# Kernel optimization log

Hardware: AMD Instinct MI355X
Metric: run time of the kernel (lower is better)

## Reference

```python
import jax, jax.numpy as jnp
import numpy as np

B, T, DIM = 1, 2048, 1024
NUM_HEADS, HEAD_DIM = 8, 128
ATTN_SCALE = 0.12


def _rms_norm(x):
    # F.rms_norm(x, x.size(-1)) with no weight; eps defaults to machine eps
    eps = jnp.asarray(jnp.finfo(x.dtype).eps, x.dtype)
    return x * jax.lax.rsqrt(jnp.mean(x * x, axis=-1, keepdims=True) + eps)


def _rotary_tables(seq_len, head_dim):
    # (1/1024) ** linspace(0,1,head_dim//4), then pad with head_dim//4 zeros
    freq = (1.0 / 1024.0) ** jnp.linspace(0.0, 1.0, head_dim // 4, dtype=jnp.float32)
    ang = jnp.concatenate([freq, jnp.zeros(head_dim // 4, jnp.float32)])  # [hd/2]
    theta = jnp.arange(seq_len, dtype=jnp.float32)[:, None] * ang[None, :]  # [T, hd/2]
    return jnp.cos(theta), jnp.sin(theta)


def _apply_rotary(x, cos, sin):
    # x: [B, T, H, hd]
    x1, x2 = jnp.split(x.astype(jnp.float32), 2, axis=-1)
    c = cos[None, :, None, :]
    s = sin[None, :, None, :]
    y1 = x1 * c + x2 * s
    y2 = -x1 * s + x2 * c
    return jnp.concatenate([y1, y2], axis=-1).astype(x.dtype)


def setup_inputs() -> dict:
    key = jax.random.key(0)
    ks = jax.random.split(key, 5)
    bound = (3.0 ** 0.5) * 0.5 * DIM ** (-0.5)
    x = jax.random.normal(ks[0], (B, T, DIM), jnp.float32)
    ve = jax.random.normal(ks[1], (B, T, NUM_HEADS * HEAD_DIM), jnp.float32)
    qkv_w = jax.random.uniform(ks[2], (3, NUM_HEADS * HEAD_DIM, DIM), jnp.float32, -bound, bound)
    lambdas = jnp.array([0.5, 0.5], jnp.float32)
    # original zero-inits c_proj; use small random weight so the output is nontrivial
    c_proj_w = jax.random.uniform(ks[3], (DIM, NUM_HEADS * HEAD_DIM), jnp.float32, -bound, bound)
    return {"x": x, "ve": ve, "qkv_w": qkv_w, "lambdas": lambdas, "c_proj_w": c_proj_w}


def reference(x, ve, qkv_w, lambdas, c_proj_w):
    Bx, Tx, D = x.shape
    H, hd = NUM_HEADS, HEAD_DIM
    # fused QKV projection: weight [3*H*hd, D]
    qkv = x @ qkv_w.reshape(3 * H * hd, D).T            # [B, T, 3*H*hd]
    qkv = qkv.reshape(Bx, Tx, 3 * H, hd)
    q, k, v = jnp.split(qkv, 3, axis=-2)                # each [B, T, H, hd]
    q, k = _rms_norm(q), _rms_norm(k)
    cos, sin = _rotary_tables(Tx, hd)
    q, k = _apply_rotary(q, cos, sin), _apply_rotary(k, cos, sin)
    v = lambdas[0] * v + lambdas[1] * ve.reshape(v.shape)
    att = jnp.einsum('bthd,bshd->bhts', q, k) * ATTN_SCALE
    causal = jnp.tril(jnp.ones((Tx, Tx), bool))
    att = jnp.where(causal[None, None], att, -jnp.inf)
    att = jax.nn.softmax(att, axis=-1)
    y = jnp.einsum('bhts,bshd->bthd', att, v).reshape(Bx, Tx, H * hd)
    return y @ c_proj_w.T
```

## Files before the change

### kernel.cpp

```cpp
#include <hip/hip_runtime.h>


typedef __attribute__((ext_vector_type(8))) short short8;
typedef __attribute__((ext_vector_type(4))) short short4b;
typedef __attribute__((ext_vector_type(4))) float fx4;
typedef __attribute__((ext_vector_type(8))) unsigned short ushort8;
typedef __attribute__((ext_vector_type(4))) unsigned short ushort4v;
typedef __attribute__((ext_vector_type(2))) unsigned short ushort2v;
typedef __attribute__((ext_vector_type(4))) float float4v;

#define T_SEQ 2048
#define NH 8
#define HD 128

__device__ __forceinline__ unsigned short f2bf(float f) {
  union { float f; unsigned u; } v; v.f = f;
  unsigned u = v.u;
  u += 0x7fffu + ((u >> 16) & 1u);
  return (unsigned short)(u >> 16);
}
__device__ __forceinline__ short bf_t(float f) {
  union { float f; unsigned u; } v; v.f = f;
  return (short)(v.u >> 16);
}
__device__ __forceinline__ float bf2f(unsigned short h) {
  union { unsigned u; float f; } v; v.u = ((unsigned)h) << 16;
  return v.f;
}

typedef __attribute__((address_space(1))) unsigned int glb_u32;
typedef __attribute__((address_space(3))) unsigned int lds_u32;
__device__ __forceinline__ void gl_lds16(const unsigned short* g, unsigned short* l) {
  __builtin_amdgcn_global_load_lds((const glb_u32*)g, (lds_u32*)l, 16, 0, 0);
}

__global__ __launch_bounds__(256) void cast3_kernel(
    const float* __restrict__ x, const float* __restrict__ w1,
    const float* __restrict__ w2, unsigned short* __restrict__ o) {
  long q = (long)blockIdx.x * 256 + threadIdx.x;
  const float* src;
  if (q < 524288)        src = x  + 4 * q;
  else if (q < 1310720)  src = w1 + 4 * (q - 524288);
  else                   src = w2 + 4 * (q - 1310720);
  float4v v = *(const float4v*)src;
  ushort4v r;
  r[0] = f2bf(v[0]); r[1] = f2bf(v[1]); r[2] = f2bf(v[2]); r[3] = f2bf(v[3]);
  *(ushort4v*)(o + 4 * q) = r;
}

template <bool OUT_BF16, int BM, int BN, int MINW>
__global__ __launch_bounds__(256, MINW) void gemm_bt4(
    const unsigned short* __restrict__ A, const unsigned short* __restrict__ B,
    void* __restrict__ Cp, int M, int N, int K) {
  constexpr int MT = BM / 32;
  constexpr int NT = BN / 32;
  constexpr int ASEG = BM / 8;
  constexpr int NLOAD = (BM + BN) / 32;
  __shared__ unsigned short a_sh[2][BM * 64];
  __shared__ unsigned short b_sh[2][BN * 64];
  const int tid = threadIdx.x;
  const int wave = tid >> 6, lane = tid & 63;
  const int ln = lane & 15, quad = lane >> 4;
  const int wm = wave & 1, wn = wave >> 1;
  const long arow0 = (long)blockIdx.y * BM;
  const long brow0 = (long)blockIdx.x * BN;

  const unsigned short* gsrc[NLOAD];
  unsigned short* ldst[NLOAD];
  int bstr[NLOAD];
  for (int i = 0; i < NLOAD; ++i) {
    int s = wave * NLOAD + i;
    int isB = s >= ASEG;
    int srel = isB ? s - ASEG : s;
    int li = srel * 64 + lane;
    int row = li >> 3, posc = li & 7;
    int c = posc ^ (row & 7);
    gsrc[i] = (isB ? B + brow0 * (long)K : A + arow0 * (long)K)
              + (long)row * K + c * 8;
    ldst[i] = (isB ? &b_sh[0][0] : &a_sh[0][0]) + srel * 512;
    bstr[i] = isB ? BN * 64 : BM * 64;
  }
  for (int i = 0; i < NLOAD; ++i) gl_lds16(gsrc[i], ldst[i]);

  fx4 acc[MT][NT] = {};
  int cur = 0;
  for (int k0 = 0; k0 < K; k0 += 64, cur ^= 1) {
    __syncthreads();
    if (k0 + 64 < K)
      for (int i = 0; i < NLOAD; ++i)
        gl_lds16(gsrc[i] + k0 + 64, ldst[i] + (cur ^ 1) * bstr[i]);
    const unsigned short* ash = &a_sh[cur][0];
    const unsigned short* bsh = &b_sh[cur][0];
    short8 af[2][MT], bfr[2][NT];
    for (int kq = 0; kq < 2; ++kq) {
      for (int mt = 0; mt < MT; ++mt) {
        int m = wm * (BM / 2) + mt * 16 + ln;
        int pos = (kq * 4 + quad) ^ (m & 7);
        af[kq][mt] = *(const short8*)&ash[m * 64 + pos * 8];
      }
      for (int nt = 0; nt < NT; ++nt) {
        int n = wn * (BN / 2) + nt * 16 + ln;
        int pos = (kq * 4 + quad) ^ (n & 7);
        bfr[kq][nt] = *(const short8*)&bsh[n * 64 + pos * 8];
      }
    }
    for (int kq = 0; kq < 2; ++kq)
      for (int mt = 0; mt < MT; ++mt)
        for (int nt = 0; nt < NT; ++nt)
          acc[mt][nt] = __builtin_amdgcn_mfma_f32_16x16x32_bf16(
              af[kq][mt], bfr[kq][nt], acc[mt][nt], 0, 0, 0);
  }
  for (int mt = 0; mt < MT; ++mt)
    for (int nt = 0; nt < NT; ++nt)
      for (int r = 0; r < 4; ++r) {
        long row = arow0 + wm * (BM / 2) + mt * 16 + quad * 4 + r;
        long col = brow0 + wn * (BN / 2) + nt * 16 + ln;
        float v = acc[mt][nt][r];
        if constexpr (OUT_BF16)
          ((unsigned short*)Cp)[row * N + col] = f2bf(v);
        else
          ((float*)Cp)[row * N + col] = v;
      }
}

__global__ __launch_bounds__(256) void prep_qkv(
    const unsigned short* __restrict__ qkv, const float* __restrict__ ve,
    const float* __restrict__ lambdas, unsigned short* __restrict__ qh,
    unsigned short* __restrict__ kh, unsigned short* __restrict__ vt) {
  __shared__ unsigned short lt[64 * 72];
  const int bx = blockIdx.x, h = blockIdx.y;
  const int tid = threadIdx.x;

  if (bx < 128) {
    const int r2 = tid >> 5, c = tid & 31;
    float ang[2];
    for (int u = 0; u < 2; ++u) {
      int dd = 2 * c + u;
      ang[u] = (dd < 32) ? exp2f(-10.0f * (float)dd / 31.0f) : 0.0f;
    }
    for (int rr = 0; rr < 2; ++rr) {
      int t = bx * 16 + rr * 8 + r2;
      float cv[2], sv[2];
      for (int u = 0; u < 2; ++u) {
        float th = (float)t * ang[u];
        sv[u] = __sinf(th); cv[u] = __cosf(th);
      }
      for (int which = 0; which < 2; ++which) {
        const unsigned short* src = qkv + (long)t * 3072 + which * 1024 + h * 128;
        ushort2v aa = *(const ushort2v*)(src + 2 * c);
        ushort2v bb = *(const ushort2v*)(src + 64 + 2 * c);
        float x1[2] = { bf2f(aa[0]), bf2f(aa[1]) };
        float x2[2] = { bf2f(bb[0]), bf2f(bb[1]) };
        float ss = x1[0]*x1[0] + x1[1]*x1[1] + x2[0]*x2[0] + x2[1]*x2[1];
        for (int off = 1; off < 32; off <<= 1) ss += __shfl_xor(ss, off);
        float rn = rsqrtf(ss * (1.0f / 128.0f) + 1.1920929e-7f);
        ushort2v o1, o2;
        for (int u = 0; u < 2; ++u) {
          float y1 = ( x1[u] * cv[u] + x2[u] * sv[u]) * rn;
          float y2 = (-x1[u] * sv[u] + x2[u] * cv[u]) * rn;
          o1[u] = f2bf(y1); o2[u] = f2bf(y2);
        }
        unsigned short* dst = (which ? kh : qh) + ((long)h * T_SEQ + t) * 128;
        *(ushort2v*)(dst + 2 * c) = o1;
        *(ushort2v*)(dst + 64 + 2 * c) = o2;
      }
    }
  } else {
    const int vb = bx - 128;
    const int tt = vb >> 1, dsub = vb & 1;
    const float l0 = lambdas[0], l1 = lambdas[1];
    const int r = tid >> 2, cb = (tid & 3) * 16;
    const unsigned short* vs = qkv + (long)(tt * 64 + r) * 3072 + 2048
                               + h * 128 + dsub * 64 + cb;
    const float* es = ve + (long)(tt * 64 + r) * 1024 + h * 128 + dsub * 64 + cb;
    ushort8 vv[2];
    for (int q = 0; q < 2; ++q) vv[q] = *(const ushort8*)(vs + 8 * q);
    float4v ee[4];
    for (int q = 0; q < 4; ++q) ee[q] = *(const float4v*)(es + 4 * q);
    for (int j = 0; j < 16; ++j) {
      float v = bf2f(vv[j >> 3][j & 7]) * l0 + ee[j >> 2][j & 3] * l1;
      lt[(cb + j) * 72 + r] = f2bf(v);
    }
    __syncthreads();
    const int d = tid >> 2, quarter = tid & 3;
    unsigned short* dst = vt + ((long)h * HD + dsub * 64 + d) * T_SEQ
                          + tt * 64 + quarter * 16;
    const unsigned short* srcl = &lt[d * 72];
    for (int g = 0; g < 4; ++g) {
      int p0 = quarter * 16 + g * 4;
      int kv0 = ((p0 >> 5) & 1) * 32 + ((p0 >> 2) & 1) * 16 + ((p0 >> 3) & 3) * 4;
      *(ushort4v*)(dst + g * 4) = *(const ushort4v*)(srcl + kv0);
    }
  }
}

#define ATT_C1 0.17312340490667562f
#define ATT_C2 23.083120654223415f

__global__ __launch_bounds__(256, 2) void attn_part(
    const unsigned short* __restrict__ qh, const unsigned short* __restrict__ kh,
    const unsigned short* __restrict__ vt, unsigned short* __restrict__ Yp,
    float* __restrict__ lp) {
  __shared__ unsigned short kbuf[2][8192];
  __shared__ unsigned short vbuf[2][8192];
  const int tid = threadIdx.x;
  const int wave = tid >> 6, lane = tid & 63;
  const int ln = lane & 15, quad = lane >> 4;
  const int qt = 15 - (int)blockIdx.x, h = blockIdx.y, ch = blockIdx.z;
  const int jmax = 2 * qt + 1;
  const int j0 = ch * 4;
  if (j0 > jmax) return;
  const int j1 = min(j0 + 3, jmax);

  int qg[2];
  short8 qf[2][4];
  for (int s = 0; s < 2; ++s) {
    qg[s] = qt * 128 + wave * 32 + s * 16 + ln;
    const unsigned short* qbase = qh + ((long)h * T_SEQ + qg[s]) * 128;
    for (int kc = 0; kc < 4; ++kc)
      qf[s][kc] = *(const short8*)(qbase + kc * 32 + quad * 8);
  }
  fx4 accy[2][8] = {};
  float l_loc[2] = {0.f, 0.f};

  const unsigned short* kg[4]; unsigned short* kl[4];
  const unsigned short* vg[4]; unsigned short* vl[4];
  for (int i = 0; i < 4; ++i) {
    int s = wave * 4 + i;
    { int li = s * 64 + lane; int row = li >> 4, posc = li & 15;
      int c = posc ^ (row & 15);
      kg[i] = kh + ((long)h * T_SEQ + row) * 128 + c * 8;
      kl[i] = &kbuf[0][s * 512]; }
    { int li = s * 64 + lane; int row = li >> 3, posc = li & 7;
      int c = posc ^ (row & 7);
      vg[i] = vt + ((long)h * HD + row) * T_SEQ + c * 8;
      vl[i] = &vbuf[0][s * 512]; }
  }
  for (int i = 0; i < 4; ++i) gl_lds16(kg[i] + (long)j0 * 8192, kl[i]);
  for (int i = 0; i < 4; ++i) gl_lds16(vg[i] + (long)j0 * 64, vl[i]);

  int cur = 0;
  for (int jt = j0; jt <= j1; ++jt, cur ^= 1) {
    __syncthreads();
    if (jt < j1) {
      int nb = (cur ^ 1) * 8192;
      for (int i = 0; i < 4; ++i) gl_lds16(kg[i] + (long)(jt + 1) * 8192, kl[i] + nb);
      for (int i = 0; i < 4; ++i) gl_lds16(vg[i] + (long)(jt + 1) * 64, vl[i] + nb);
    }
    const unsigned short* kb_ = &kbuf[cur][0];
    fx4 s4[2][4];
    for (int kt = 0; kt < 4; ++kt) {
      s4[0][kt] = fx4{0.f, 0.f, 0.f, 0.f};
      s4[1][kt] = fx4{0.f, 0.f, 0.f, 0.f};
      for (int kc = 0; kc < 4; ++kc) {
        int pos = (kc * 4 + quad) ^ ln;
        short8 kf = *(const short8*)&kb_[(kt * 16 + ln) * 128 + pos * 8];
        s4[0][kt] = __builtin_amdgcn_mfma_f32_16x16x32_bf16(kf, qf[0][kc], s4[0][kt], 0, 0, 0);
        s4[1][kt] = __builtin_amdgcn_mfma_f32_16x16x32_bf16(kf, qf[1][kc], s4[1][kt], 0, 0, 0);
      }
    }
    short4b pb[2][4];
    for (int s = 0; s < 2; ++s)
      for (int kt = 0; kt < 4; ++kt) {
        int kvb = jt * 64 + kt * 16 + quad * 4;
        float p[4];
        for (int r = 0; r < 4; ++r)
          p[r] = exp2f(fmaf(s4[s][kt][r], ATT_C1, -ATT_C2));
        if (jt * 64 + kt * 16 + 15 > qt * 128 + wave * 32 + s * 16) {
          for (int r = 0; r < 4; ++r) if (kvb + r > qg[s]) p[r] = 0.f;
        }
        l_loc[s] += (p[0] + p[1]) + (p[2] + p[3]);
        pb[s][kt] = short4b{ bf_t(p[0]), bf_t(p[1]), bf_t(p[2]), bf_t(p[3]) };
      }
    const unsigned short* vb_ = &vbuf[cur][0];
    for (int kh2 = 0; kh2 < 2; ++kh2) {
      for (int dt = 0; dt < 8; ++dt) {
        int row = dt * 16 + ln;
        int pos = (kh2 * 4 + quad) ^ (ln & 7);
        short8 va = *(const short8*)&vb_[row * 64 + pos * 8];
        short4b va0 = { va[0], va[1], va[2], va[3] };
        short4b va1 = { va[4], va[5], va[6], va[7] };
        for (int s = 0; s < 2; ++s) {
          accy[s][dt] = __builtin_amdgcn_mfma_f32_16x16x16bf16_1k(
              va0, pb[s][kh2 * 2], accy[s][dt], 0, 0, 0);
          accy[s][dt] = __builtin_amdgcn_mfma_f32_16x16x16bf16_1k(
              va1, pb[s][kh2 * 2 + 1], accy[s][dt], 0, 0, 0);
        }
      }
    }
  }

  int cbase = qt + ((qt - 1) * (qt - 1)) / 4;
  const long pp = (long)(h * 72 + cbase + ch);
  for (int s = 0; s < 2; ++s) {
    float l = l_loc[s];
    l += __shfl_xor(l, 16);
    l += __shfl_xor(l, 32);
    int q = wave * 32 + s * 16 + ln;
    if (quad == 0) lp[pp * 128 + q] = l;
    unsigned short* yb = Yp + pp * 16384 + (long)q * 128;
    for (int dt = 0; dt < 8; ++dt) {
      ushort4v o;
      for (int r = 0; r < 4; ++r) o[r] = f2bf(accy[s][dt][r]);
      *(ushort4v*)(yb + dt * 16 + quad * 4) = o;
    }
  }
}

__global__ __launch_bounds__(256) void attn_combine(
    const unsigned short* __restrict__ Yp, const float* __restrict__ lp,
    unsigned short* __restrict__ y) {
  const int bx = blockIdx.x, h = blockIdx.y;
  const int tid = threadIdx.x;
  const int row = bx * 16 + (tid >> 4);
  const int cb  = (tid & 15) * 8;
  const int qt = row >> 7;
  const int r128 = row & 127;
  const int nc = (qt >> 1) + 1;
  const int cbase = qt + ((qt - 1) * (qt - 1)) / 4;
  float acc[8];
  for (int j = 0; j < 8; ++j) acc[j] = 0.f;
  float ltot = 0.f;
  for (int c = 0; c < nc; ++c) {
    long pp = (long)(h * 72 + cbase + c);
    const unsigned short* ys = Yp + pp * 16384 + (long)r128 * 128 + cb;
    ltot += lp[pp * 128 + r128];
    ushort8 v = *(const ushort8*)ys;
    for (int j = 0; j < 8; ++j) acc[j] += bf2f(v[j]);
  }
  float inv = 1.f / ltot;
  unsigned short* dst = y + (long)row * 1024 + h * 128 + cb;
  ushort8 o;
  for (int j = 0; j < 8; ++j) o[j] = f2bf(acc[j] * inv);
  *(ushort8*)dst = o;
}

extern "C" void kernel_launch(void* const* d_in, const int* in_sizes, int n_in,
                              void* d_out, int out_size, void* d_ws, size_t ws_size,
                              hipStream_t stream) {
  const float* x       = (const float*)d_in[0];
  const float* ve      = (const float*)d_in[1];
  const float* qkv_w   = (const float*)d_in[2];
  const float* lambdas = (const float*)d_in[3];
  const float* c_proj  = (const float*)d_in[4];
  char* ws = (char*)d_ws;
  unsigned short* qkv_bf = (unsigned short*)(ws);
  unsigned short* x_bf   = (unsigned short*)(ws + 12582912);
  unsigned short* wqkv   = (unsigned short*)(ws + 16777216);
  unsigned short* wproj  = (unsigned short*)(ws + 23068672);
  unsigned short* qhat   = (unsigned short*)(ws + 25165824);
  unsigned short* khat   = (unsigned short*)(ws + 29360128);
  unsigned short* vtb    = (unsigned short*)(ws + 33554432);
  unsigned short* ybf    = (unsigned short*)(ws + 37748736);
  unsigned short* Yp     = (unsigned short*)(ws);
  float*          lpart  = (float*)(ws + 18874368);
  float* out = (float*)d_out;

  cast3_kernel<<<6144, 256, 0, stream>>>(x, qkv_w, c_proj, x_bf);
  gemm_bt4<true, 64, 128, 3><<<dim3(24, 32), 256, 0, stream>>>(x_bf, wqkv, qkv_bf, 2048, 3072, 1024);
  prep_qkv<<<dim3(192, 8), 256, 0, stream>>>(qkv_bf, ve, lambdas, qhat, khat, vtb);
  attn_part<<<dim3(16, 8, 8), 256, 0, stream>>>(qhat, khat, vtb, Yp, lpart);
  attn_combine<<<dim3(128, 8), 256, 0, stream>>>(Yp, lpart, ybf);
  gemm_bt4<false, 32, 64, 4><<<dim3(16, 64), 256, 0, stream>>>(ybf, wproj, out, 2048, 1024, 1024);
}
```

Measured before the change: 168.5 us.

## Pre-swizzle V into MFMA fragment layout and load directly to registers

The V-prep kernel now writes V in a per-tile, per-fragment layout so each lane can read its MFMA operand with contiguous 16-byte global loads. The attention kernel drops the V shared-memory double buffer and loads 16 V fragments per tile straight into registers. Launch bounds rise from 2 to 3 blocks per SM. This removes LDS traffic and LDS capacity for V, in exchange for more register pressure and global-load latency that is not hidden by an async prefetch.

```diff
diff --git a/kernel.cpp b/kernel.cpp
--- a/kernel.cpp
+++ b/kernel.cpp
@@ -167,12 +167,12 @@
     }
   } else {
     const int vb = bx - 128;
-    const int tt = vb >> 1, dsub = vb & 1;
+    const int jt = vb >> 1, dsub = vb & 1;
     const float l0 = lambdas[0], l1 = lambdas[1];
     const int r = tid >> 2, cb = (tid & 3) * 16;
-    const unsigned short* vs = qkv + (long)(tt * 64 + r) * 3072 + 2048
+    const unsigned short* vs = qkv + (long)(jt * 64 + r) * 3072 + 2048
                                + h * 128 + dsub * 64 + cb;
-    const float* es = ve + (long)(tt * 64 + r) * 1024 + h * 128 + dsub * 64 + cb;
+    const float* es = ve + (long)(jt * 64 + r) * 1024 + h * 128 + dsub * 64 + cb;
     ushort8 vv[2];
     for (int q = 0; q < 2; ++q) vv[q] = *(const ushort8*)(vs + 8 * q);
     float4v ee[4];
@@ -182,27 +182,27 @@
       lt[(cb + j) * 72 + r] = f2bf(v);
     }
     __syncthreads();
-    const int d = tid >> 2, quarter = tid & 3;
-    unsigned short* dst = vt + ((long)h * HD + dsub * 64 + d) * T_SEQ
-                          + tt * 64 + quarter * 16;
-    const unsigned short* srcl = &lt[d * 72];
-    for (int g = 0; g < 4; ++g) {
-      int p0 = quarter * 16 + g * 4;
-      int kv0 = ((p0 >> 5) & 1) * 32 + ((p0 >> 2) & 1) * 16 + ((p0 >> 3) & 3) * 4;
-      *(ushort4v*)(dst + g * 4) = *(const ushort4v*)(srcl + kv0);
-    }
+    const int dl = tid >> 2, quarter = tid & 3;
+    const int d = dsub * 64 + dl;
+    const int dt = d >> 4, lnn = d & 15;
+    const int kh2 = quarter >> 1, half = quarter & 1;
+    unsigned short* dstb = vt + (((long)h * 32 + jt) * 16 + kh2 * 8 + dt) * 512
+                           + half * 4;
+    const unsigned short* srcl = &lt[dl * 72];
+    for (int g = 0; g < 4; ++g)
+      *(ushort4v*)(dstb + (g * 16 + lnn) * 8) =
+          *(const ushort4v*)(srcl + quarter * 16 + g * 4);
   }
 }
 
 #define ATT_C1 0.17312340490667562f
 #define ATT_C2 23.083120654223415f
 
-__global__ __launch_bounds__(256, 2) void attn_part(
+__global__ __launch_bounds__(256, 3) void attn_part(
     const unsigned short* __restrict__ qh, const unsigned short* __restrict__ kh,
     const unsigned short* __restrict__ vt, unsigned short* __restrict__ Yp,
     float* __restrict__ lp) {
   __shared__ unsigned short kbuf[2][8192];
-  __shared__ unsigned short vbuf[2][8192];
   const int tid = threadIdx.x;
   const int wave = tid >> 6, lane = tid & 63;
   const int ln = lane & 15, quad = lane >> 4;
@@ -224,29 +224,28 @@
   float l_loc[2] = {0.f, 0.f};
 
   const unsigned short* kg[4]; unsigned short* kl[4];
-  const unsigned short* vg[4]; unsigned short* vl[4];
   for (int i = 0; i < 4; ++i) {
     int s = wave * 4 + i;
-    { int li = s * 64 + lane; int row = li >> 4, posc = li & 15;
-      int c = posc ^ (row & 15);
-      kg[i] = kh + ((long)h * T_SEQ + row) * 128 + c * 8;
-      kl[i] = &kbuf[0][s * 512]; }
-    { int li = s * 64 + lane; int row = li >> 3, posc = li & 7;
-      int c = posc ^ (row & 7);
-      vg[i] = vt + ((long)h * HD + row) * T_SEQ + c * 8;
-      vl[i] = &vbuf[0][s * 512]; }
+    int li = s * 64 + lane; int row = li >> 4, posc = li & 15;
+    int c = posc ^ (row & 15);
+    kg[i] = kh + ((long)h * T_SEQ + row) * 128 + c * 8;
+    kl[i] = &kbuf[0][s * 512];
   }
   for (int i = 0; i < 4; ++i) gl_lds16(kg[i] + (long)j0 * 8192, kl[i]);
-  for (int i = 0; i < 4; ++i) gl_lds16(vg[i] + (long)j0 * 64, vl[i]);
+
+  const unsigned short* vlane = vt + ((long)h * 32) * 8192 + lane * 8;
 
   int cur = 0;
   for (int jt = j0; jt <= j1; ++jt, cur ^= 1) {
     __syncthreads();
-    if (jt < j1) {
-      int nb = (cur ^ 1) * 8192;
-      for (int i = 0; i < 4; ++i) gl_lds16(kg[i] + (long)(jt + 1) * 8192, kl[i] + nb);
-      for (int i = 0; i < 4; ++i) gl_lds16(vg[i] + (long)(jt + 1) * 64, vl[i] + nb);
-    }
+    if (jt < j1)
+      for (int i = 0; i < 4; ++i)
+        gl_lds16(kg[i] + (long)(jt + 1) * 8192, kl[i] + (cur ^ 1) * 8192);
+    const unsigned short* vb_ = vlane + (long)jt * 8192;
+    short8 vf[16];
+#pragma unroll
+    for (int f = 0; f < 16; ++f) vf[f] = *(const short8*)(vb_ + f * 512);
+
     const unsigned short* kb_ = &kbuf[cur][0];
     fx4 s4[2][4];
     for (int kt = 0; kt < 4; ++kt) {
@@ -272,12 +271,11 @@
         l_loc[s] += (p[0] + p[1]) + (p[2] + p[3]);
         pb[s][kt] = short4b{ bf_t(p[0]), bf_t(p[1]), bf_t(p[2]), bf_t(p[3]) };
       }
-    const unsigned short* vb_ = &vbuf[cur][0];
+#pragma unroll
     for (int kh2 = 0; kh2 < 2; ++kh2) {
+#pragma unroll
       for (int dt = 0; dt < 8; ++dt) {
-        int row = dt * 16 + ln;
-        int pos = (kh2 * 4 + quad) ^ (ln & 7);
-        short8 va = *(const short8*)&vb_[row * 64 + pos * 8];
+        short8 va = vf[kh2 * 8 + dt];
         short4b va0 = { va[0], va[1], va[2], va[3] };
         short4b va1 = { va[4], va[5], va[6], va[7] };
         for (int s = 0; s < 2; ++s) {
```

Result: slower. 243.5 us (+44.5%).
